# Kernel tuning notes

Measured on AMD Instinct MI355X. Metric: run time of the kernel, lower is better.

## Reference

```python
import jax, jax.numpy as jnp
import numpy as np
import math

B, S, D, H, FF = 4, 2048, 1024, 16, 4096
DH = D // H
EPS = 1e-6


def setup_inputs() -> dict:
    key = jax.random.key(0)
    ks = jax.random.split(key, 12)
    s = 0.02
    inp = {
        "x": jax.random.normal(ks[0], (B, S, D), dtype=jnp.float32),
        "mask": jax.random.randint(ks[1], (B, 1, S, S), 0, 2, dtype=jnp.int32),
        # torch Linear y = x @ W.T + b; we store W already transposed as [in, out]
        "Wq": jax.random.normal(ks[2], (D, D), dtype=jnp.float32) * s,
        "bq": jnp.zeros((D,), jnp.float32),
        "Wk": jax.random.normal(ks[3], (D, D), dtype=jnp.float32) * s,
        "bk": jnp.zeros((D,), jnp.float32),
        "Wv": jax.random.normal(ks[4], (D, D), dtype=jnp.float32) * s,
        "bv": jnp.zeros((D,), jnp.float32),
        "Wo": jax.random.normal(ks[5], (D, D), dtype=jnp.float32) * s,
        "bo": jnp.zeros((D,), jnp.float32),
        "ln1_g": jnp.ones((D,), jnp.float32),
        "ln1_b": jnp.zeros((D,), jnp.float32),
        "W1": jax.random.normal(ks[6], (D, FF), dtype=jnp.float32) * s,
        "b1": jnp.zeros((FF,), jnp.float32),
        "W2": jax.random.normal(ks[7], (FF, D), dtype=jnp.float32) * s,
        "b2": jnp.zeros((D,), jnp.float32),
        "ln2_g": jnp.ones((D,), jnp.float32),
        "ln2_b": jnp.zeros((D,), jnp.float32),
    }
    return inp


def _layer_norm(x, g, b):
    m = jnp.mean(x, axis=-1, keepdims=True)
    v = jnp.mean(jnp.square(x - m), axis=-1, keepdims=True)
    return (x - m) * jax.lax.rsqrt(v + EPS) * g + b


def reference(x, mask, Wq, bq, Wk, bk, Wv, bv, Wo, bo,
              ln1_g, ln1_b, W1, b1, W2, b2, ln2_g, ln2_b):
    # ---- multi-head self-attention (dropout = identity, eval mode) ----
    def split_heads(t):  # [B,S,D] -> [B,H,S,DH]
        return t.reshape(B, S, H, DH).transpose(0, 2, 1, 3)

    q = split_heads(x @ Wq + bq)
    k = split_heads(x @ Wk + bk)
    v = split_heads(x @ Wv + bv)

    scores = jnp.einsum("bhqd,bhkd->bhqk", q, k) / math.sqrt(DH)
    scores = jnp.where(mask == 0, jnp.float32(-1e9), scores)
    attn = jax.nn.softmax(scores, axis=-1)
    out = jnp.einsum("bhqk,bhkd->bhqd", attn, v)
    out = out.transpose(0, 2, 1, 3).reshape(B, S, D)
    attn_out = out @ Wo + bo

    # ---- sublayer 1: x + LayerNorm(attn_out)  (post-applied LN, faithful) ----
    x = x + _layer_norm(attn_out, ln1_g, ln1_b)

    # ---- FFN with exact GELU ----
    ff = jax.nn.gelu(x @ W1 + b1, approximate=False) @ W2 + b2

    # ---- sublayer 2 ----
    x = x + _layer_norm(ff, ln2_g, ln2_b)
    return x
```

## Files before the change

### kernel.cpp

```cpp
#include <hip/hip_runtime.h>
#include <hip/hip_bf16.h>

#define BDIM 4
#define SDIM 2048
#define DDIM 1024
#define HDIM 16
#define FFDIM 4096
#define MROWS (BDIM*SDIM)

using bf16 = __hip_bfloat16;
typedef __attribute__((ext_vector_type(8))) short short8;
typedef __attribute__((ext_vector_type(4))) float f32x4;

__device__ __forceinline__ f32x4 mfma16(short8 a, short8 b, f32x4 c) {
  return __builtin_amdgcn_mfma_f32_16x16x32_bf16(a, b, c, 0, 0, 0);
}

__device__ __forceinline__ void gll16(const void* g, void* l) {
  __builtin_amdgcn_global_load_lds((const __attribute__((address_space(1))) void*)g,
                                   (__attribute__((address_space(3))) void*)l, 16, 0, 0);
}

template<int EPI>
__global__ __launch_bounds__(256)
void gemm_bt(const bf16* __restrict__ A, const bf16* __restrict__ Bt,
             const float* __restrict__ bias0, const float* __restrict__ bias1,
             const float* __restrict__ bias2,
             void* __restrict__ Cout, int K, int N)
{
  __shared__ bf16 As[128*32];
  __shared__ bf16 Bs[128*32];
  const int tid  = threadIdx.x;
  const int wave = tid >> 6;
  const int lane = tid & 63;
  const int llo  = lane & 15, lhi = lane >> 4;
  const int row0 = blockIdx.y * 128;
  const int col0 = blockIdx.x * 128;
  const int wm = wave >> 1, wn = wave & 1;

  f32x4 acc[4][4];
#pragma unroll
  for (int i = 0; i < 4; i++)
#pragma unroll
    for (int j = 0; j < 4; j++) acc[i][j] = (f32x4){0.f, 0.f, 0.f, 0.f};

  const int c0 = wave * 2, c1 = wave * 2 + 1;
  const size_t arow0 = (size_t)(row0 + c0*16 + (lane >> 2)) * K;
  const size_t arow1 = (size_t)(row0 + c1*16 + (lane >> 2)) * K;
  const size_t brow0 = (size_t)(col0 + c0*16 + (lane >> 2)) * K;
  const size_t brow1 = (size_t)(col0 + c1*16 + (lane >> 2)) * K;
  const int colb = (lane & 3) * 8;

  const int nkt = K >> 5;
  for (int kt = 0; kt < nkt; ++kt) {
    __syncthreads();
    const int kofs = kt * 32 + colb;
    gll16(A  + arow0 + kofs, As + c0*512);
    gll16(A  + arow1 + kofs, As + c1*512);
    gll16(Bt + brow0 + kofs, Bs + c0*512);
    gll16(Bt + brow1 + kofs, Bs + c1*512);
    __syncthreads();
    short8 af[4], bfr[4];
#pragma unroll
    for (int mi = 0; mi < 4; mi++)
      af[mi] = *(const short8*)(As + (wm*64 + mi*16 + llo)*32 + lhi*8);
#pragma unroll
    for (int ni = 0; ni < 4; ni++)
      bfr[ni] = *(const short8*)(Bs + (wn*64 + ni*16 + llo)*32 + lhi*8);
#pragma unroll
    for (int mi = 0; mi < 4; mi++)
#pragma unroll
      for (int ni = 0; ni < 4; ni++)
        acc[mi][ni] = mfma16(af[mi], bfr[ni], acc[mi][ni]);
  }

#pragma unroll
  for (int mi = 0; mi < 4; mi++) {
#pragma unroll
    for (int ni = 0; ni < 4; ni++) {
      const int col = col0 + wn*64 + ni*16 + llo;
      float bv;
      if (EPI == 1) {
        const int which = col >> 10, win = col & 1023;
        const float* bp = (which == 0) ? bias0 : ((which == 1) ? bias1 : bias2);
        bv = bp[win];
      } else {
        bv = bias0[col];
      }
#pragma unroll
      for (int r = 0; r < 4; r++) {
        const int row = row0 + wm*64 + mi*16 + lhi*4 + r;
        float v = acc[mi][ni][r] + bv;
        if (EPI == 0) {
          ((float*)Cout)[(size_t)row * N + col] = v;
        } else if (EPI == 1) {
          const int which = col >> 10, win = col & 1023;
          const int h = win >> 6, dh = win & 63;
          const int b = row >> 11, s = row & 2047;
          ((bf16*)Cout)[((((size_t)which*BDIM + b)*HDIM + h)*SDIM + s)*64 + dh] =
              __float2bfloat16(v);
        } else {
          float gl = 0.5f * v * (1.f + erff(v * 0.70710678118654752f));
          ((bf16*)Cout)[(size_t)row * N + col] = __float2bfloat16(gl);
        }
      }
    }
  }
}

__global__ __launch_bounds__(256)
void attn_fwd(const bf16* __restrict__ qkv, const bf16* __restrict__ maskb,
              bf16* __restrict__ Obuf)
{
  __shared__ bf16 Ks[64*64];
  __shared__ bf16 Vt[64*64];
  __shared__ bf16 Ms[64*64];
  __shared__ bf16 Ps[4][16*64];

  const int tid  = threadIdx.x;
  const int wave = tid >> 6, lane = tid & 63;
  const int llo  = lane & 15, lhi = lane >> 4;
  const int bh = blockIdx.y;
  const int b = bh >> 4, h = bh & 15;
  const int q0 = blockIdx.x * 64;

  const bf16* Qp = qkv + (((size_t)0*BDIM + b)*HDIM + h) * (size_t)SDIM * 64;
  const bf16* Kp = qkv + (((size_t)1*BDIM + b)*HDIM + h) * (size_t)SDIM * 64;
  const bf16* Vp = qkv + (((size_t)2*BDIM + b)*HDIM + h) * (size_t)SDIM * 64;

  short8 qf[2];
  {
    const bf16* qrow = Qp + (size_t)(q0 + wave*16 + llo) * 64;
    qf[0] = *(const short8*)(qrow + lhi*8);
    qf[1] = *(const short8*)(qrow + 32 + lhi*8);
  }

  f32x4 o[4];
#pragma unroll
  for (int n = 0; n < 4; n++) o[n] = (f32x4){0.f, 0.f, 0.f, 0.f};
  float mrun[4], lrun[4];
#pragma unroll
  for (int r = 0; r < 4; r++) { mrun[r] = -INFINITY; lrun[r] = 0.f; }

  const int vrow = tid >> 2, vc0 = (tid & 3) * 16;
  const int c0 = wave * 2, c1 = wave * 2 + 1;

  for (int kt = 0; kt < SDIM/64; ++kt) {
    const int k0 = kt * 64;
    f32x4 vreg0 = *(const f32x4*)(Vp + (size_t)(k0 + vrow)*64 + vc0);
    f32x4 vreg1 = *(const f32x4*)(Vp + (size_t)(k0 + vrow)*64 + vc0 + 8);
    __syncthreads();
    gll16(Kp + (size_t)(k0 + c0*8 + (lane >> 3))*64 + (lane & 7)*8, Ks + c0*512);
    gll16(Kp + (size_t)(k0 + c1*8 + (lane >> 3))*64 + (lane & 7)*8, Ks + c1*512);
    gll16(maskb + ((size_t)b*SDIM + q0 + c0*8 + (lane >> 3))*SDIM + k0 + (lane & 7)*8,
          Ms + c0*512);
    gll16(maskb + ((size_t)b*SDIM + q0 + c1*8 + (lane >> 3))*SDIM + k0 + (lane & 7)*8,
          Ms + c1*512);
    const bf16* v0 = (const bf16*)&vreg0;
    const bf16* v1 = (const bf16*)&vreg1;
#pragma unroll
    for (int j = 0; j < 8; j++) Vt[(vc0 + j)*64 + vrow] = v0[j];
#pragma unroll
    for (int j = 0; j < 8; j++) Vt[(vc0 + 8 + j)*64 + vrow] = v1[j];
    __syncthreads();

    float sv[4][4];
#pragma unroll
    for (int n = 0; n < 4; n++) {
      short8 kf0 = *(const short8*)(Ks + (n*16 + llo)*64 + lhi*8);
      short8 kf1 = *(const short8*)(Ks + (n*16 + llo)*64 + 32 + lhi*8);
      f32x4 z = (f32x4){0.f, 0.f, 0.f, 0.f};
      z = mfma16(qf[0], kf0, z);
      z = mfma16(qf[1], kf1, z);
#pragma unroll
      for (int r = 0; r < 4; r++)
        sv[n][r] = z[r]*0.125f +
            __bfloat162float(Ms[(wave*16 + lhi*4 + r)*64 + n*16 + llo]);
    }
    float mnew[4], scale[4];
#pragma unroll
    for (int r = 0; r < 4; r++) {
      float rm = fmaxf(fmaxf(sv[0][r], sv[1][r]), fmaxf(sv[2][r], sv[3][r]));
      rm = fmaxf(rm, __shfl_xor(rm, 1));
      rm = fmaxf(rm, __shfl_xor(rm, 2));
      rm = fmaxf(rm, __shfl_xor(rm, 4));
      rm = fmaxf(rm, __shfl_xor(rm, 8));
      mnew[r] = fmaxf(mrun[r], rm);
      scale[r] = __expf(mrun[r] - mnew[r]);
      mrun[r] = mnew[r];
    }
    float rsum[4] = {0.f, 0.f, 0.f, 0.f};
#pragma unroll
    for (int n = 0; n < 4; n++)
#pragma unroll
      for (int r = 0; r < 4; r++) {
        float p = __expf(sv[n][r] - mnew[r]);
        sv[n][r] = p;
        rsum[r] += p;
      }
#pragma unroll
    for (int r = 0; r < 4; r++) {
      float rs = rsum[r];
      rs += __shfl_xor(rs, 1);
      rs += __shfl_xor(rs, 2);
      rs += __shfl_xor(rs, 4);
      rs += __shfl_xor(rs, 8);
      lrun[r] = lrun[r]*scale[r] + rs;
    }
#pragma unroll
    for (int n = 0; n < 4; n++)
#pragma unroll
      for (int r = 0; r < 4; r++) o[n][r] *= scale[r];
#pragma unroll
    for (int n = 0; n < 4; n++)
#pragma unroll
      for (int r = 0; r < 4; r++)
        Ps[wave][(lhi*4 + r)*64 + n*16 + llo] = __float2bfloat16(sv[n][r]);
#pragma unroll
    for (int kk = 0; kk < 2; kk++) {
      short8 pf = *(const short8*)(&Ps[wave][llo*64 + kk*32 + lhi*8]);
#pragma unroll
      for (int n = 0; n < 4; n++) {
        short8 vf = *(const short8*)(Vt + (n*16 + llo)*64 + kk*32 + lhi*8);
        o[n] = mfma16(pf, vf, o[n]);
      }
    }
  }

#pragma unroll
  for (int n = 0; n < 4; n++)
#pragma unroll
    for (int r = 0; r < 4; r++) {
      float v = o[n][r] / lrun[r];
      const int row = q0 + wave*16 + lhi*4 + r;
      const int col = h*64 + n*16 + llo;
      Obuf[((size_t)b*SDIM + row)*DDIM + col] = __float2bfloat16(v);
    }
}

template<bool WB>
__global__ __launch_bounds__(256)
void add_ln(const float* __restrict__ resid, const float* __restrict__ y,
            const float* __restrict__ gam, const float* __restrict__ bet,
            float* __restrict__ outf, bf16* __restrict__ outb)
{
  __shared__ float red[4];
  const int row = blockIdx.x;
  const int t = threadIdx.x;
  float4 v = ((const float4*)(y + (size_t)row*DDIM))[t];
  float s = v.x + v.y + v.z + v.w;
#pragma unroll
  for (int off = 1; off < 64; off <<= 1) s += __shfl_xor(s, off);
  if ((t & 63) == 0) red[t >> 6] = s;
  __syncthreads();
  const float mean = (red[0]+red[1]+red[2]+red[3]) * (1.f/DDIM);
  const float dx = v.x-mean, dy = v.y-mean, dz = v.z-mean, dw = v.w-mean;
  float sq = dx*dx + dy*dy + dz*dz + dw*dw;
#pragma unroll
  for (int off = 1; off < 64; off <<= 1) sq += __shfl_xor(sq, off);
  __syncthreads();
  if ((t & 63) == 0) red[t >> 6] = sq;
  __syncthreads();
  const float var = (red[0]+red[1]+red[2]+red[3]) * (1.f/DDIM);
  const float rst = rsqrtf(var + 1e-6f);
  const float4 g  = ((const float4*)gam)[t];
  const float4 bb = ((const float4*)bet)[t];
  const float4 rv = ((const float4*)(resid + (size_t)row*DDIM))[t];
  float4 ov;
  ov.x = rv.x + dx*rst*g.x + bb.x;
  ov.y = rv.y + dy*rst*g.y + bb.y;
  ov.z = rv.z + dz*rst*g.z + bb.z;
  ov.w = rv.w + dw*rst*g.w + bb.w;
  ((float4*)(outf + (size_t)row*DDIM))[t] = ov;
  if (WB) {
    bf16* ob = outb + (size_t)row*DDIM + t*4;
    ob[0] = __float2bfloat16(ov.x);
    ob[1] = __float2bfloat16(ov.y);
    ob[2] = __float2bfloat16(ov.z);
    ob[3] = __float2bfloat16(ov.w);
  }
}

__global__ __launch_bounds__(256)
void transpose_cast(const float* __restrict__ in, bf16* __restrict__ out,
                    int R, int C)
{
  __shared__ float tile[32][33];
  const int x = threadIdx.x & 31, y = threadIdx.x >> 5;
  const int c0 = blockIdx.x * 32, r0 = blockIdx.y * 32;
#pragma unroll
  for (int i = 0; i < 32; i += 8)
    tile[y + i][x] = in[(size_t)(r0 + y + i)*C + c0 + x];
  __syncthreads();
#pragma unroll
  for (int i = 0; i < 32; i += 8)
    out[(size_t)(c0 + y + i)*R + r0 + x] = __float2bfloat16(tile[x][y + i]);
}

__global__ __launch_bounds__(256)
void cast_to_bf16(const float* __restrict__ in, bf16* __restrict__ out, int n4)
{
  const int i = blockIdx.x * 256 + threadIdx.x;
  if (i < n4) {
    float4 v = ((const float4*)in)[i];
    bf16* o = out + (size_t)i*4;
    o[0] = __float2bfloat16(v.x);
    o[1] = __float2bfloat16(v.y);
    o[2] = __float2bfloat16(v.z);
    o[3] = __float2bfloat16(v.w);
  }
}

__global__ __launch_bounds__(256)
void mask_bias_kernel(const int* __restrict__ mask, bf16* __restrict__ bias, int n4)
{
  const int i = blockIdx.x * 256 + threadIdx.x;
  if (i < n4) {
    int4 m = ((const int4*)mask)[i];
    bf16* o = bias + (size_t)i*4;
    const bf16 neg = __float2bfloat16(-1e9f);
    const bf16 zer = __float2bfloat16(0.f);
    o[0] = (m.x == 0) ? neg : zer;
    o[1] = (m.y == 0) ? neg : zer;
    o[2] = (m.z == 0) ? neg : zer;
    o[3] = (m.w == 0) ? neg : zer;
  }
}

extern "C" void kernel_launch(void* const* d_in, const int* in_sizes, int n_in,
                              void* d_out, int out_size, void* d_ws, size_t ws_size,
                              hipStream_t stream)
{
  (void)in_sizes; (void)n_in; (void)out_size; (void)ws_size;
  const float* x    = (const float*)d_in[0];
  const int*   mask = (const int*)d_in[1];
  const float* Wq   = (const float*)d_in[2];
  const float* bq   = (const float*)d_in[3];
  const float* Wk   = (const float*)d_in[4];
  const float* bk   = (const float*)d_in[5];
  const float* Wv   = (const float*)d_in[6];
  const float* bv   = (const float*)d_in[7];
  const float* Wo   = (const float*)d_in[8];
  const float* bo   = (const float*)d_in[9];
  const float* ln1g = (const float*)d_in[10];
  const float* ln1b = (const float*)d_in[11];
  const float* W1   = (const float*)d_in[12];
  const float* b1   = (const float*)d_in[13];
  const float* W2   = (const float*)d_in[14];
  const float* b2   = (const float*)d_in[15];
  const float* ln2g = (const float*)d_in[16];
  const float* ln2b = (const float*)d_in[17];
  float* out = (float*)d_out;

  char* ws = (char*)d_ws;
  bf16* xb    = (bf16*)(ws + 0);
  bf16* Wqkvt = (bf16*)(ws + 16777216);
  bf16* Wot   = (bf16*)(ws + 23068672);
  bf16* W1t   = (bf16*)(ws + 25165824);
  bf16* W2t   = (bf16*)(ws + 33554432);
  bf16* maskb = (bf16*)(ws + 41943040);
  bf16* qkv   = (bf16*)(ws + 75497472);
  bf16* obuf  = (bf16*)(ws + 125829120);
  float* aproj = (float*)(ws + 142606336);
  float* x1f   = (float*)(ws + 176160768);
  bf16* x1b = xb;
  bf16* h1  = qkv;
  float* ffb = (float*)maskb;

  cast_to_bf16<<<dim3(MROWS*DDIM/4/256), 256, 0, stream>>>(x, xb, MROWS*DDIM/4);
  transpose_cast<<<dim3(32, 32), 256, 0, stream>>>(Wq, Wqkvt, 1024, 1024);
  transpose_cast<<<dim3(32, 32), 256, 0, stream>>>(Wk, Wqkvt + 1024*1024, 1024, 1024);
  transpose_cast<<<dim3(32, 32), 256, 0, stream>>>(Wv, Wqkvt + 2*1024*1024, 1024, 1024);
  transpose_cast<<<dim3(32, 32), 256, 0, stream>>>(Wo, Wot, 1024, 1024);
  transpose_cast<<<dim3(FFDIM/32, 32), 256, 0, stream>>>(W1, W1t, 1024, FFDIM);
  transpose_cast<<<dim3(32, FFDIM/32), 256, 0, stream>>>(W2, W2t, FFDIM, 1024);
  mask_bias_kernel<<<dim3(BDIM*SDIM*SDIM/4/256), 256, 0, stream>>>(
      mask, maskb, BDIM*SDIM*SDIM/4);

  gemm_bt<1><<<dim3(3072/128, MROWS/128), 256, 0, stream>>>(
      xb, Wqkvt, bq, bk, bv, qkv, 1024, 3072);
  attn_fwd<<<dim3(SDIM/64, BDIM*HDIM), 256, 0, stream>>>(qkv, maskb, obuf);
  gemm_bt<0><<<dim3(1024/128, MROWS/128), 256, 0, stream>>>(
      obuf, Wot, bo, nullptr, nullptr, aproj, 1024, 1024);
  add_ln<true><<<dim3(MROWS), 256, 0, stream>>>(x, aproj, ln1g, ln1b, x1f, x1b);
  gemm_bt<2><<<dim3(FFDIM/128, MROWS/128), 256, 0, stream>>>(
      x1b, W1t, b1, nullptr, nullptr, h1, 1024, FFDIM);
  gemm_bt<0><<<dim3(1024/128, MROWS/128), 256, 0, stream>>>(
      h1, W2t, b2, nullptr, nullptr, ffb, FFDIM, 1024);
  add_ln<false><<<dim3(MROWS), 256, 0, stream>>>(x1f, ffb, ln2g, ln2b, out, nullptr);
}
```

Baseline: 941.2 us.

## Bit-pack attention mask, pre-transpose V in QKV epilogue, swizzle LDS layouts

Replaces the bf16 additive mask buffer with a 1-bit-per-element mask built by wave ballots, so attention reads 64 mask bits per row per tile instead of 64 bf16 values, and the mask-staging LDS buffer goes away. The QKV GEMM epilogue now writes V already transposed as packed 4-element stores, so attention loads V directly with async global-to-LDS copies instead of a register transpose scattered into LDS. XOR swizzles are added to the GEMM, K, V and P LDS tiles to reduce bank conflicts. The main costs are the extra bit extraction per score and the strided transposed-V stores in the GEMM epilogue.

```diff
diff --git a/kernel.cpp b/kernel.cpp
--- a/kernel.cpp
+++ b/kernel.cpp
@@ -10,6 +10,7 @@
 
 using bf16 = __hip_bfloat16;
 typedef __attribute__((ext_vector_type(8))) short short8;
+typedef __attribute__((ext_vector_type(4))) short short4v;
 typedef __attribute__((ext_vector_type(4))) float f32x4;
 
 __device__ __forceinline__ f32x4 mfma16(short8 a, short8 b, f32x4 c) {
@@ -49,7 +50,9 @@
   const size_t arow1 = (size_t)(row0 + c1*16 + (lane >> 2)) * K;
   const size_t brow0 = (size_t)(col0 + c0*16 + (lane >> 2)) * K;
   const size_t brow1 = (size_t)(col0 + c1*16 + (lane >> 2)) * K;
-  const int colb = (lane & 3) * 8;
+  const int colb = (((lane & 3) ^ ((lane >> 2) & 3))) * 8;
+  const int rslot = ( 0);
+  (void)rslot;
 
   const int nkt = K >> 5;
   for (int kt = 0; kt < nkt; ++kt) {
@@ -61,12 +64,13 @@
     gll16(Bt + brow1 + kofs, Bs + c1*512);
     __syncthreads();
     short8 af[4], bfr[4];
+    const int rsw = ((lhi ^ (llo & 3)) * 8);
 #pragma unroll
     for (int mi = 0; mi < 4; mi++)
-      af[mi] = *(const short8*)(As + (wm*64 + mi*16 + llo)*32 + lhi*8);
+      af[mi] = *(const short8*)(As + (wm*64 + mi*16 + llo)*32 + rsw);
 #pragma unroll
     for (int ni = 0; ni < 4; ni++)
-      bfr[ni] = *(const short8*)(Bs + (wn*64 + ni*16 + llo)*32 + lhi*8);
+      bfr[ni] = *(const short8*)(Bs + (wn*64 + ni*16 + llo)*32 + rsw);
 #pragma unroll
     for (int mi = 0; mi < 4; mi++)
 #pragma unroll
@@ -87,21 +91,41 @@
       } else {
         bv = bias0[col];
       }
-#pragma unroll
-      for (int r = 0; r < 4; r++) {
-        const int row = row0 + wm*64 + mi*16 + lhi*4 + r;
-        float v = acc[mi][ni][r] + bv;
-        if (EPI == 0) {
-          ((float*)Cout)[(size_t)row * N + col] = v;
-        } else if (EPI == 1) {
-          const int which = col >> 10, win = col & 1023;
-          const int h = win >> 6, dh = win & 63;
+      if (EPI == 1) {
+        const int which = col >> 10, win = col & 1023;
+        const int h = win >> 6, dh = win & 63;
+        if (which < 2) {
+#pragma unroll
+          for (int r = 0; r < 4; r++) {
+            const int row = row0 + wm*64 + mi*16 + lhi*4 + r;
+            const int b = row >> 11, s = row & 2047;
+            float v = acc[mi][ni][r] + bv;
+            ((bf16*)Cout)[((((size_t)which*BDIM + b)*HDIM + h)*SDIM + s)*64 + dh] =
+                __float2bfloat16(v);
+          }
+        } else {
+          const int row = row0 + wm*64 + mi*16 + lhi*4;
           const int b = row >> 11, s = row & 2047;
-          ((bf16*)Cout)[((((size_t)which*BDIM + b)*HDIM + h)*SDIM + s)*64 + dh] =
-              __float2bfloat16(v);
-        } else {
-          float gl = 0.5f * v * (1.f + erff(v * 0.70710678118654752f));
-          ((bf16*)Cout)[(size_t)row * N + col] = __float2bfloat16(gl);
+          short4v pk;
+#pragma unroll
+          for (int r = 0; r < 4; r++) {
+            bf16 t = __float2bfloat16(acc[mi][ni][r] + bv);
+            pk[r] = *(short*)&t;
+          }
+          bf16* vt = (bf16*)Cout + (size_t)2*BDIM*HDIM*SDIM*64;
+          *(short4v*)(vt + (((size_t)b*HDIM + h)*64 + dh)*SDIM + s) = pk;
+        }
+      } else {
+#pragma unroll
+        for (int r = 0; r < 4; r++) {
+          const int row = row0 + wm*64 + mi*16 + lhi*4 + r;
+          float v = acc[mi][ni][r] + bv;
+          if (EPI == 0) {
+            ((float*)Cout)[(size_t)row * N + col] = v;
+          } else {
+            float gl = 0.5f * v * (1.f + erff(v * 0.70710678118654752f));
+            ((bf16*)Cout)[(size_t)row * N + col] = __float2bfloat16(gl);
+          }
         }
       }
     }
@@ -109,12 +133,12 @@
 }
 
 __global__ __launch_bounds__(256)
-void attn_fwd(const bf16* __restrict__ qkv, const bf16* __restrict__ maskb,
+void attn_fwd(const bf16* __restrict__ qkv,
+              const unsigned long long* __restrict__ mbits,
               bf16* __restrict__ Obuf)
 {
   __shared__ bf16 Ks[64*64];
-  __shared__ bf16 Vt[64*64];
-  __shared__ bf16 Ms[64*64];
+  __shared__ bf16 Vs[64*64];
   __shared__ bf16 Ps[4][16*64];
 
   const int tid  = threadIdx.x;
@@ -124,9 +148,10 @@
   const int b = bh >> 4, h = bh & 15;
   const int q0 = blockIdx.x * 64;
 
-  const bf16* Qp = qkv + (((size_t)0*BDIM + b)*HDIM + h) * (size_t)SDIM * 64;
-  const bf16* Kp = qkv + (((size_t)1*BDIM + b)*HDIM + h) * (size_t)SDIM * 64;
-  const bf16* Vp = qkv + (((size_t)2*BDIM + b)*HDIM + h) * (size_t)SDIM * 64;
+  const bf16* Qp  = qkv + ((size_t)b*HDIM + h) * (size_t)SDIM * 64;
+  const bf16* Kp  = qkv + ((size_t)(BDIM*HDIM) + b*HDIM + h) * (size_t)SDIM * 64;
+  const bf16* Vtp = qkv + (size_t)2*BDIM*HDIM*SDIM*64
+                        + ((size_t)b*HDIM + h) * (size_t)64 * SDIM;
 
   short8 qf[2];
   {
@@ -142,40 +167,37 @@
 #pragma unroll
   for (int r = 0; r < 4; r++) { mrun[r] = -INFINITY; lrun[r] = 0.f; }
 
-  const int vrow = tid >> 2, vc0 = (tid & 3) * 16;
   const int c0 = wave * 2, c1 = wave * 2 + 1;
+  const int srow = lane >> 3;
+  const int scol = ((lane & 7) ^ srow) * 8;
+  const size_t mrow = ((size_t)b*SDIM + q0 + wave*16 + lhi*4) * 32;
 
   for (int kt = 0; kt < SDIM/64; ++kt) {
     const int k0 = kt * 64;
-    f32x4 vreg0 = *(const f32x4*)(Vp + (size_t)(k0 + vrow)*64 + vc0);
-    f32x4 vreg1 = *(const f32x4*)(Vp + (size_t)(k0 + vrow)*64 + vc0 + 8);
     __syncthreads();
-    gll16(Kp + (size_t)(k0 + c0*8 + (lane >> 3))*64 + (lane & 7)*8, Ks + c0*512);
-    gll16(Kp + (size_t)(k0 + c1*8 + (lane >> 3))*64 + (lane & 7)*8, Ks + c1*512);
-    gll16(maskb + ((size_t)b*SDIM + q0 + c0*8 + (lane >> 3))*SDIM + k0 + (lane & 7)*8,
-          Ms + c0*512);
-    gll16(maskb + ((size_t)b*SDIM + q0 + c1*8 + (lane >> 3))*SDIM + k0 + (lane & 7)*8,
-          Ms + c1*512);
-    const bf16* v0 = (const bf16*)&vreg0;
-    const bf16* v1 = (const bf16*)&vreg1;
-#pragma unroll
-    for (int j = 0; j < 8; j++) Vt[(vc0 + j)*64 + vrow] = v0[j];
-#pragma unroll
-    for (int j = 0; j < 8; j++) Vt[(vc0 + 8 + j)*64 + vrow] = v1[j];
+    gll16(Kp + (size_t)(k0 + c0*8 + srow)*64 + scol, Ks + c0*512);
+    gll16(Kp + (size_t)(k0 + c1*8 + srow)*64 + scol, Ks + c1*512);
+    gll16(Vtp + (size_t)(c0*8 + srow)*SDIM + k0 + scol, Vs + c0*512);
+    gll16(Vtp + (size_t)(c1*8 + srow)*SDIM + k0 + scol, Vs + c1*512);
+    unsigned long long mw[4];
+#pragma unroll
+    for (int r = 0; r < 4; r++) mw[r] = mbits[mrow + (size_t)r*32 + kt];
     __syncthreads();
 
     float sv[4][4];
 #pragma unroll
     for (int n = 0; n < 4; n++) {
-      short8 kf0 = *(const short8*)(Ks + (n*16 + llo)*64 + lhi*8);
-      short8 kf1 = *(const short8*)(Ks + (n*16 + llo)*64 + 32 + lhi*8);
+      const int krow = (n*16 + llo) * 64;
+      const int sw   = llo & 7;
+      short8 kf0 = *(const short8*)(Ks + krow + ((lhi ^ sw) * 8));
+      short8 kf1 = *(const short8*)(Ks + krow + (((4 | lhi) ^ sw) * 8));
       f32x4 z = (f32x4){0.f, 0.f, 0.f, 0.f};
       z = mfma16(qf[0], kf0, z);
       z = mfma16(qf[1], kf1, z);
 #pragma unroll
       for (int r = 0; r < 4; r++)
         sv[n][r] = z[r]*0.125f +
-            __bfloat162float(Ms[(wave*16 + lhi*4 + r)*64 + n*16 + llo]);
+            (((mw[r] >> (n*16 + llo)) & 1ull) ? 0.f : -1e9f);
     }
     float mnew[4], scale[4];
 #pragma unroll
@@ -214,14 +236,18 @@
 #pragma unroll
     for (int n = 0; n < 4; n++)
 #pragma unroll
-      for (int r = 0; r < 4; r++)
-        Ps[wave][(lhi*4 + r)*64 + n*16 + llo] = __float2bfloat16(sv[n][r]);
+      for (int r = 0; r < 4; r++) {
+        const int prow = lhi*4 + r;
+        const int slot = (n*2 + (llo >> 3)) ^ (prow & 7);
+        Ps[wave][prow*64 + slot*8 + (llo & 7)] = __float2bfloat16(sv[n][r]);
+      }
 #pragma unroll
     for (int kk = 0; kk < 2; kk++) {
-      short8 pf = *(const short8*)(&Ps[wave][llo*64 + kk*32 + lhi*8]);
+      const int sl = ((kk*4 + lhi) ^ (llo & 7)) * 8;
+      short8 pf = *(const short8*)(&Ps[wave][llo*64 + sl]);
 #pragma unroll
       for (int n = 0; n < 4; n++) {
-        short8 vf = *(const short8*)(Vt + (n*16 + llo)*64 + kk*32 + lhi*8);
+        short8 vf = *(const short8*)(Vs + (n*16 + llo)*64 + sl);
         o[n] = mfma16(pf, vf, o[n]);
       }
     }
@@ -312,19 +338,14 @@
 }
 
 __global__ __launch_bounds__(256)
-void mask_bias_kernel(const int* __restrict__ mask, bf16* __restrict__ bias, int n4)
-{
-  const int i = blockIdx.x * 256 + threadIdx.x;
-  if (i < n4) {
-    int4 m = ((const int4*)mask)[i];
-    bf16* o = bias + (size_t)i*4;
-    const bf16 neg = __float2bfloat16(-1e9f);
-    const bf16 zer = __float2bfloat16(0.f);
-    o[0] = (m.x == 0) ? neg : zer;
-    o[1] = (m.y == 0) ? neg : zer;
-    o[2] = (m.z == 0) ? neg : zer;
-    o[3] = (m.w == 0) ? neg : zer;
-  }
+void mask_bits_kernel(const int* __restrict__ mask,
+                      unsigned long long* __restrict__ bits)
+{
+  const int wid = blockIdx.x * 4 + (threadIdx.x >> 6);
+  const int lane = threadIdx.x & 63;
+  const int m = mask[(size_t)wid * 64 + lane];
+  const unsigned long long bal = __ballot(m != 0);
+  if (lane == 0) bits[wid] = bal;
 }
 
 extern "C" void kernel_launch(void* const* d_in, const int* in_sizes, int n_in,
@@ -358,14 +379,14 @@
   bf16* Wot   = (bf16*)(ws + 23068672);
   bf16* W1t   = (bf16*)(ws + 25165824);
   bf16* W2t   = (bf16*)(ws + 33554432);
-  bf16* maskb = (bf16*)(ws + 41943040);
+  unsigned long long* mbits = (unsigned long long*)(ws + 41943040);
   bf16* qkv   = (bf16*)(ws + 75497472);
   bf16* obuf  = (bf16*)(ws + 125829120);
   float* aproj = (float*)(ws + 142606336);
   float* x1f   = (float*)(ws + 176160768);
   bf16* x1b = xb;
   bf16* h1  = qkv;
-  float* ffb = (float*)maskb;
+  float* ffb = (float*)(ws + 41943040);
 
   cast_to_bf16<<<dim3(MROWS*DDIM/4/256), 256, 0, stream>>>(x, xb, MROWS*DDIM/4);
   transpose_cast<<<dim3(32, 32), 256, 0, stream>>>(Wq, Wqkvt, 1024, 1024);
@@ -374,12 +395,11 @@
   transpose_cast<<<dim3(32, 32), 256, 0, stream>>>(Wo, Wot, 1024, 1024);
   transpose_cast<<<dim3(FFDIM/32, 32), 256, 0, stream>>>(W1, W1t, 1024, FFDIM);
   transpose_cast<<<dim3(32, FFDIM/32), 256, 0, stream>>>(W2, W2t, FFDIM, 1024);
-  mask_bias_kernel<<<dim3(BDIM*SDIM*SDIM/4/256), 256, 0, stream>>>(
-      mask, maskb, BDIM*SDIM*SDIM/4);
+  mask_bits_kernel<<<dim3(BDIM*SDIM*SDIM/64/4), 256, 0, stream>>>(mask, mbits);
 
   gemm_bt<1><<<dim3(3072/128, MROWS/128), 256, 0, stream>>>(
       xb, Wqkvt, bq, bk, bv, qkv, 1024, 3072);
-  attn_fwd<<<dim3(SDIM/64, BDIM*HDIM), 256, 0, stream>>>(qkv, maskb, obuf);
+  attn_fwd<<<dim3(SDIM/64, BDIM*HDIM), 256, 0, stream>>>(qkv, mbits, obuf);
   gemm_bt<0><<<dim3(1024/128, MROWS/128), 256, 0, stream>>>(
       obuf, Wot, bo, nullptr, nullptr, aproj, 1024, 1024);
   add_ln<true><<<dim3(MROWS), 256, 0, stream>>>(x, aproj, ln1g, ln1b, x1f, x1b);
```

Measured after the change: 845.1 us. 10.2% less time.
